# Kernel tuning notes

Measured on AMD Instinct MI355X. Metric: run time of the kernel, lower is better.

## Reference

```python
import jax, jax.numpy as jnp
import numpy as np

B, T, HID = 2, 1024, 2048
NH, NKV, HD = 16, 4, 128
L, INTER = 4, 5632
EPS = 1e-6


def _rope_tables(key):
    inv_freq = 1.0 / (10000.0 ** (jnp.arange(0, HD, 2, dtype=jnp.float32) / HD))  # [HD/2]
    pos = jnp.arange(T, dtype=jnp.float32)
    freqs = pos[:, None] * inv_freq[None, :]          # [T, HD/2]
    emb = jnp.concatenate([freqs, freqs], axis=-1)    # [T, HD]
    cos = jnp.broadcast_to(jnp.cos(emb)[None], (B, T, HD))
    sin = jnp.broadcast_to(jnp.sin(emb)[None], (B, T, HD))
    return cos, sin


def setup_inputs() -> dict:
    key = jax.random.key(0)
    ks = jax.random.split(key, 12)
    std = 0.02
    cos, sin = _rope_tables(key)
    return {
        "hidden_states": jax.random.normal(ks[0], (B, T, HID), jnp.float32),
        "cos": cos,
        "sin": sin,
        "qw": jax.random.normal(ks[1], (L, NH * HD, HID), jnp.float32) * std,
        "qb": jnp.zeros((L, NH * HD), jnp.float32),
        "kw": jax.random.normal(ks[2], (L, NKV * HD, HID), jnp.float32) * std,
        "kb": jnp.zeros((L, NKV * HD), jnp.float32),
        "vw": jax.random.normal(ks[3], (L, NKV * HD, HID), jnp.float32) * std,
        "vb": jnp.zeros((L, NKV * HD), jnp.float32),
        "ow": jax.random.normal(ks[4], (L, HID, NH * HD), jnp.float32) * std,
        "gatew": jax.random.normal(ks[5], (L, INTER, HID), jnp.float32) * std,
        "upw": jax.random.normal(ks[6], (L, INTER, HID), jnp.float32) * std,
        "downw": jax.random.normal(ks[7], (L, HID, INTER), jnp.float32) * std,
        "ln1w": jnp.ones((L, HID), jnp.float32),
        "ln2w": jnp.ones((L, HID), jnp.float32),
        "normw": jnp.ones((HID,), jnp.float32),
    }


def _rmsnorm(x, w):
    xf = x.astype(jnp.float32)
    var = jnp.mean(xf * xf, axis=-1, keepdims=True)
    return (w * (xf * jax.lax.rsqrt(var + EPS))).astype(x.dtype)


def _rotate_half(x):
    x1, x2 = x[..., : HD // 2], x[..., HD // 2:]
    return jnp.concatenate([-x2, x1], axis=-1)


def _layer(x, cos, sin, mask, qw, qb, kw, kb, vw, vb, ow, gw, uw, dw, l1, l2):
    # --- attention (PreNorm) ---
    h = _rmsnorm(x, l1)
    q = (h @ qw.T + qb).reshape(B, T, NH, HD).transpose(0, 2, 1, 3)    # [B,NH,T,D]
    k = (h @ kw.T + kb).reshape(B, T, NKV, HD).transpose(0, 2, 1, 3)   # [B,NKV,T,D]
    v = (h @ vw.T + vb).reshape(B, T, NKV, HD).transpose(0, 2, 1, 3)
    c, s = cos[:, None], sin[:, None]                                  # [B,1,T,D]
    q = q * c + _rotate_half(q) * s
    k = k * c + _rotate_half(k) * s
    rep = NH // NKV
    k = jnp.repeat(k, rep, axis=1)                                     # GQA repeat_kv
    v = jnp.repeat(v, rep, axis=1)
    scores = jnp.einsum("bhqd,bhkd->bhqk", q, k) / (HD ** 0.5) + mask
    attn = jax.nn.softmax(scores.astype(jnp.float32), axis=-1).astype(q.dtype)
    ao = jnp.einsum("bhqk,bhkd->bhqd", attn, v)
    ao = ao.transpose(0, 2, 1, 3).reshape(B, T, NH * HD) @ ow.T
    x = x + ao
    # --- SwiGLU MLP (PreNorm) ---
    h = _rmsnorm(x, l2)
    x = x + (jax.nn.silu(h @ gw.T) * (h @ uw.T)) @ dw.T
    return x


def reference(hidden_states, cos, sin, qw, qb, kw, kb, vw, vb, ow,
              gatew, upw, downw, ln1w, ln2w, normw):
    min_val = jnp.finfo(hidden_states.dtype).min
    qpos = jnp.arange(T)
    mask = jnp.where(qpos[None, :] > qpos[:, None], min_val, 0.0).astype(hidden_states.dtype)
    mask = mask[None, None]  # [1,1,T,T]
    x = hidden_states
    for i in range(L):
        x = _layer(x, cos, sin, mask, qw[i], qb[i], kw[i], kb[i], vw[i], vb[i],
                   ow[i], gatew[i], upw[i], downw[i], ln1w[i], ln2w[i])
    return _rmsnorm(x, normw)
```

## Files before the change

kernel.cpp:

```cpp
#include <hip/hip_runtime.h>


typedef __attribute__((ext_vector_type(8))) __bf16 bf16x8;
typedef __attribute__((ext_vector_type(4))) float f32x4;
typedef __attribute__((ext_vector_type(4))) unsigned short u16x4;

#define DEV __device__ __forceinline__
#define BARRIER() asm volatile("s_barrier" ::: "memory")

#define NTOK 2048
#define HIDDIM 2048
#define KVDIM 512
#define HDIM 128
#define INTERDIM 5632

DEV unsigned short f2bf(float f) {
  union { float f; unsigned u; } a; a.f = f;
  unsigned r = a.u + 0x7fffu + ((a.u >> 16) & 1u);
  return (unsigned short)(r >> 16);
}
DEV float bf2f(unsigned short h) {
  union { unsigned u; float f; } a; a.u = ((unsigned)h) << 16;
  return a.f;
}
DEV unsigned short f2h(float f) {
  union { _Float16 h; unsigned short u; } c; c.h = (_Float16)f; return c.u;
}
DEV float h2f(unsigned short u) {
  union { unsigned short u; _Float16 h; } c; c.u = u; return (float)c.h;
}
DEV void gload_lds16(const void* g, void* l) {
  __builtin_amdgcn_global_load_lds(
      (const __attribute__((address_space(1))) unsigned int*)(g),
      (__attribute__((address_space(3))) unsigned int*)(l), 16, 0, 0);
}

__global__ __launch_bounds__(256) void cvt_kernel(
    const float* __restrict__ in, unsigned short* __restrict__ out, int n8) {
  const int i = blockIdx.x * 256 + threadIdx.x;
  if (i >= n8) return;
  const f32x4* p = reinterpret_cast<const f32x4*>(in) + (size_t)i * 2;
  const f32x4 a = p[0], b = p[1];
  bf16x8 o;
  o[0] = (__bf16)a.x; o[1] = (__bf16)a.y; o[2] = (__bf16)a.z; o[3] = (__bf16)a.w;
  o[4] = (__bf16)b.x; o[5] = (__bf16)b.y; o[6] = (__bf16)b.z; o[7] = (__bf16)b.w;
  *reinterpret_cast<bf16x8*>(out + (size_t)i * 8) = o;
}

__global__ __launch_bounds__(256) void cvt_gu(
    const float* __restrict__ gw, const float* __restrict__ uw,
    unsigned short* __restrict__ out) {
  const int i = blockIdx.x * 256 + threadIdx.x;
  const int row = i >> 8, g8 = i & 255;
  const int t = row >> 8, sub = row & 255;
  const float* src = (sub < 128)
                         ? gw + (size_t)(t * 128 + sub) * 2048
                         : uw + (size_t)(t * 128 + sub - 128) * 2048;
  const f32x4* p = reinterpret_cast<const f32x4*>(src) + (size_t)g8 * 2;
  const f32x4 a = p[0], b = p[1];
  bf16x8 o;
  o[0] = (__bf16)a.x; o[1] = (__bf16)a.y; o[2] = (__bf16)a.z; o[3] = (__bf16)a.w;
  o[4] = (__bf16)b.x; o[5] = (__bf16)b.y; o[6] = (__bf16)b.z; o[7] = (__bf16)b.w;
  *reinterpret_cast<bf16x8*>(out + (size_t)row * 2048 + g8 * 8) = o;
}

template <int OUTF32>
__global__ __launch_bounds__(256) void rmsnorm_kernel(
    const float* __restrict__ x, const float* __restrict__ w,
    void* __restrict__ outp) {
  const int row = blockIdx.x, tid = threadIdx.x;
  const int lane = tid & 63, wave = tid >> 6;
  const float* xr = x + (size_t)row * HIDDIM;
  f32x4 v0 = *reinterpret_cast<const f32x4*>(xr + tid * 4);
  f32x4 v1 = *reinterpret_cast<const f32x4*>(xr + 1024 + tid * 4);
  float ss = v0.x * v0.x + v0.y * v0.y + v0.z * v0.z + v0.w * v0.w +
             v1.x * v1.x + v1.y * v1.y + v1.z * v1.z + v1.w * v1.w;
#pragma unroll
  for (int off = 1; off < 64; off <<= 1) ss += __shfl_xor(ss, off, 64);
  __shared__ float red[4];
  if (lane == 0) red[wave] = ss;
  __syncthreads();
  ss = red[0] + red[1] + red[2] + red[3];
  const float rs = rsqrtf(ss * (1.0f / 2048.0f) + 1e-6f);
  f32x4 w0 = *reinterpret_cast<const f32x4*>(w + tid * 4);
  f32x4 w1 = *reinterpret_cast<const f32x4*>(w + 1024 + tid * 4);
  if (OUTF32) {
    float* o = (float*)outp + (size_t)row * HIDDIM;
    f32x4 o0, o1;
    o0.x = v0.x * rs * w0.x; o0.y = v0.y * rs * w0.y;
    o0.z = v0.z * rs * w0.z; o0.w = v0.w * rs * w0.w;
    o1.x = v1.x * rs * w1.x; o1.y = v1.y * rs * w1.y;
    o1.z = v1.z * rs * w1.z; o1.w = v1.w * rs * w1.w;
    *reinterpret_cast<f32x4*>(o + tid * 4) = o0;
    *reinterpret_cast<f32x4*>(o + 1024 + tid * 4) = o1;
  } else {
    unsigned short* o = (unsigned short*)outp + (size_t)row * HIDDIM;
    u16x4 p0, p1;
    p0.x = f2bf(v0.x * rs * w0.x); p0.y = f2bf(v0.y * rs * w0.y);
    p0.z = f2bf(v0.z * rs * w0.z); p0.w = f2bf(v0.w * rs * w0.w);
    p1.x = f2bf(v1.x * rs * w1.x); p1.y = f2bf(v1.y * rs * w1.y);
    p1.z = f2bf(v1.z * rs * w1.z); p1.w = f2bf(v1.w * rs * w1.w);
    *reinterpret_cast<u16x4*>(o + tid * 4) = p0;
    *reinterpret_cast<u16x4*>(o + 1024 + tid * 4) = p1;
  }
}

template <int KS, int OUTF32>
__global__ __launch_bounds__(256) void reduce_rms(
    float* __restrict__ x, const unsigned short* __restrict__ p, size_t zs,
    const float* __restrict__ w, void* __restrict__ outp) {
  const int row = blockIdx.x, tid = threadIdx.x;
  const int lane = tid & 63, wave = tid >> 6;
  float* xr = x + (size_t)row * HIDDIM;
  f32x4 v0 = *reinterpret_cast<const f32x4*>(xr + tid * 4);
  f32x4 v1 = *reinterpret_cast<const f32x4*>(xr + 1024 + tid * 4);
#pragma unroll
  for (int s = 0; s < KS; ++s) {
    const unsigned short* pr = p + (size_t)s * zs + (size_t)row * HIDDIM;
    u16x4 a = *reinterpret_cast<const u16x4*>(pr + tid * 4);
    u16x4 b = *reinterpret_cast<const u16x4*>(pr + 1024 + tid * 4);
    v0.x += bf2f(a.x); v0.y += bf2f(a.y); v0.z += bf2f(a.z); v0.w += bf2f(a.w);
    v1.x += bf2f(b.x); v1.y += bf2f(b.y); v1.z += bf2f(b.z); v1.w += bf2f(b.w);
  }
  *reinterpret_cast<f32x4*>(xr + tid * 4) = v0;
  *reinterpret_cast<f32x4*>(xr + 1024 + tid * 4) = v1;
  float ss = v0.x * v0.x + v0.y * v0.y + v0.z * v0.z + v0.w * v0.w +
             v1.x * v1.x + v1.y * v1.y + v1.z * v1.z + v1.w * v1.w;
#pragma unroll
  for (int off = 1; off < 64; off <<= 1) ss += __shfl_xor(ss, off, 64);
  __shared__ float red[4];
  if (lane == 0) red[wave] = ss;
  __syncthreads();
  ss = red[0] + red[1] + red[2] + red[3];
  const float rs = rsqrtf(ss * (1.0f / 2048.0f) + 1e-6f);
  f32x4 w0 = *reinterpret_cast<const f32x4*>(w + tid * 4);
  f32x4 w1 = *reinterpret_cast<const f32x4*>(w + 1024 + tid * 4);
  if (OUTF32) {
    float* o = (float*)outp + (size_t)row * HIDDIM;
    f32x4 o0, o1;
    o0.x = v0.x * rs * w0.x; o0.y = v0.y * rs * w0.y;
    o0.z = v0.z * rs * w0.z; o0.w = v0.w * rs * w0.w;
    o1.x = v1.x * rs * w1.x; o1.y = v1.y * rs * w1.y;
    o1.z = v1.z * rs * w1.z; o1.w = v1.w * rs * w1.w;
    *reinterpret_cast<f32x4*>(o + tid * 4) = o0;
    *reinterpret_cast<f32x4*>(o + 1024 + tid * 4) = o1;
  } else {
    unsigned short* o = (unsigned short*)outp + (size_t)row * HIDDIM;
    u16x4 p0, p1;
    p0.x = f2bf(v0.x * rs * w0.x); p0.y = f2bf(v0.y * rs * w0.y);
    p0.z = f2bf(v0.z * rs * w0.z); p0.w = f2bf(v0.w * rs * w0.w);
    p1.x = f2bf(v1.x * rs * w1.x); p1.y = f2bf(v1.y * rs * w1.y);
    p1.z = f2bf(v1.z * rs * w1.z); p1.w = f2bf(v1.w * rs * w1.w);
    *reinterpret_cast<u16x4*>(o + tid * 4) = p0;
    *reinterpret_cast<u16x4*>(o + 1024 + tid * 4) = p1;
  }
}

struct G16Setup {
  const unsigned short* srcp0;
  const unsigned short* srcp1;
  int ldsc0, ldsc1;
};

DEV G16Setup g16_setup(const unsigned short* A, const unsigned short* W,
                       int K, int m0, int n0, int t0, int wave, int lane) {
  const int c0 = wave * 2, c1 = wave * 2 + 1;
  const int rA = lane >> 2;
  const int cg = (((lane & 3) ^ ((lane >> 3) & 3))) * 8;
  G16Setup s;
  const unsigned short* gb[4] = {
      A + (size_t)m0 * K, A + (size_t)(m0 + 128) * K,
      W + (size_t)n0 * K, W + (size_t)(n0 + 128) * K};
  s.srcp0 = gb[c0 >> 3] + (size_t)((c0 & 7) * 16 + rA) * K + cg +
            (size_t)t0 * 32;
  s.srcp1 = gb[c1 >> 3] + (size_t)((c1 & 7) * 16 + rA) * K + cg +
            (size_t)t0 * 32;
  s.ldsc0 = c0 * 512;
  s.ldsc1 = c1 * 512;
  return s;
}

#define G16STAGE(st_, tt_, c_)                                                \
  do {                                                                        \
    gload_lds16(st_.srcp0 + (size_t)(tt_)*32, &lds[(c_)*16384 + st_.ldsc0]);  \
    gload_lds16(st_.srcp1 + (size_t)(tt_)*32, &lds[(c_)*16384 + st_.ldsc1]);  \
  } while (0)

#define G16LDA(mi_, c_)                                                       \
  (*reinterpret_cast<const bf16x8*>(                                          \
      &lds[(c_)*16384 + (wm >> 1) * 4096 +                                    \
           (((wm & 1) * 64) + (mi_)*16 + fr) * 32 +                           \
           ((lq ^ ((fr >> 1) & 3))) * 8]))
#define G16LDB(ni_, c_)                                                       \
  (*reinterpret_cast<const bf16x8*>(                                          \
      &lds[(c_)*16384 + (2 + (wn >> 1)) * 4096 +                              \
           (((wn & 1) * 64) + (ni_)*16 + fr) * 32 +                           \
           ((lq ^ ((fr >> 1) & 3))) * 8]))

#define G16KLOOP(NT_)                                                         \
  G16STAGE(st, 0, 0);                                                         \
  for (int t = 0; t < (NT_); ++t) {                                           \
    const int c = t & 1;                                                      \
    if (t + 1 < (NT_)) {                                                      \
      G16STAGE(st, t + 1, c ^ 1);                                             \
      asm volatile("s_waitcnt vmcnt(2)" ::: "memory");                        \
    } else {                                                                  \
      asm volatile("s_waitcnt vmcnt(0)" ::: "memory");                        \
    }                                                                         \
    BARRIER();                                                                \
    bf16x8 aF[4], bF[4];                                                      \
    bF[0] = G16LDB(0, c); bF[1] = G16LDB(1, c);                               \
    bF[2] = G16LDB(2, c); bF[3] = G16LDB(3, c);                               \
    aF[0] = G16LDA(0, c); aF[1] = G16LDA(1, c);                               \
    aF[2] = G16LDA(2, c); aF[3] = G16LDA(3, c);                               \
    __builtin_amdgcn_s_setprio(1);                                            \
    _Pragma("unroll") for (int ni = 0; ni < 4; ++ni)                          \
        _Pragma("unroll") for (int mi = 0; mi < 4; ++mi)                      \
            acc[mi][ni] = __builtin_amdgcn_mfma_f32_16x16x32_bf16(            \
                aF[mi], bF[ni], acc[mi][ni], 0, 0, 0);                        \
    __builtin_amdgcn_s_setprio(0);                                            \
    __builtin_amdgcn_sched_barrier(0);                                        \
    BARRIER();                                                                \
  }

__global__ __launch_bounds__(1024) void gemm16w(
    const unsigned short* __restrict__ A, const unsigned short* __restrict__ W,
    unsigned short* __restrict__ outp, int K, int ldo, int kt_split,
    int kt_tot, size_t zstride) {
  __shared__ unsigned short lds[32768];
  const int tid = threadIdx.x, lane = tid & 63, wave = tid >> 6;
  const int fr = lane & 15, lq = lane >> 4;
  const int wm = wave >> 2, wn = wave & 3;

  int bx = blockIdx.x, by = blockIdx.y;
  {
    const int nbx = gridDim.x, nwg = nbx * gridDim.y;
    const int lin = by * nbx + bx, cpx = nwg >> 3;
    const int swz = (lin & 7) * cpx + (lin >> 3);
    bx = swz % nbx; by = swz / nbx;
  }
  const int m0 = by * 256, n0 = bx * 256;
  const int bz = blockIdx.z;
  const int t0 = bz * kt_split;
  int NT = kt_tot - t0; if (NT > kt_split) NT = kt_split;

  G16Setup st = g16_setup(A, W, K, m0, n0, t0, wave, lane);
  f32x4 acc[4][4] = {};
  G16KLOOP(NT);

  const int r0 = lq * 4;
#pragma unroll
  for (int mi = 0; mi < 4; ++mi)
#pragma unroll
    for (int ni = 0; ni < 4; ++ni)
#pragma unroll
      for (int r = 0; r < 4; ++r) {
        const int gm = m0 + wm * 64 + mi * 16 + r0 + r;
        const int gn = n0 + wn * 64 + ni * 16 + fr;
        outp[(size_t)bz * zstride + (size_t)gm * ldo + gn] =
            f2bf(acc[mi][ni][r]);
      }
}

__global__ __launch_bounds__(1024) void gemm_gu16(
    const unsigned short* __restrict__ A, const unsigned short* __restrict__ W,
    unsigned short* __restrict__ act) {
  __shared__ unsigned short lds[32768];
  const int tid = threadIdx.x, lane = tid & 63, wave = tid >> 6;
  const int fr = lane & 15, lq = lane >> 4;
  const int wm = wave >> 2, wn = wave & 3;
  const int K = 2048;

  int bx = blockIdx.x, by = blockIdx.y;
  {
    const int nbx = gridDim.x, nwg = nbx * gridDim.y;
    const int lin = by * nbx + bx, cpx = nwg >> 3;
    const int swz = (lin & 7) * cpx + (lin >> 3);
    bx = swz % nbx; by = swz / nbx;
  }
  const int m0 = by * 256, n0 = bx * 256;

  G16Setup st = g16_setup(A, W, K, m0, n0, 0, wave, lane);
  f32x4 acc[4][4] = {};
  G16KLOOP(64);

  float* fl = reinterpret_cast<float*>(lds);
  const int r0 = lq * 4;
#pragma unroll 1
  for (int rd = 0; rd < 4; ++rd) {
    __syncthreads();
    if (wm == rd && wn < 2) {
#pragma unroll
      for (int mi = 0; mi < 4; ++mi)
#pragma unroll
        for (int ni = 0; ni < 4; ++ni)
#pragma unroll
          for (int r = 0; r < 4; ++r)
            fl[(mi * 16 + r0 + r) * 128 + wn * 64 + ni * 16 + fr] =
                acc[mi][ni][r];
    }
    __syncthreads();
    if (wm == rd && wn >= 2) {
      const int wnu = wn - 2;
#pragma unroll
      for (int mi = 0; mi < 4; ++mi)
#pragma unroll
        for (int ni = 0; ni < 4; ++ni)
#pragma unroll
          for (int r = 0; r < 4; ++r) {
            const int mrow = mi * 16 + r0 + r;
            const float g = fl[mrow * 128 + wnu * 64 + ni * 16 + fr];
            const float s = g / (1.f + __expf(-g));
            const int gm = m0 + wm * 64 + mrow;
            const int ic = (n0 >> 1) + wnu * 64 + ni * 16 + fr;
            act[(size_t)gm * INTERDIM + ic] = f2bf(s * acc[mi][ni][r]);
          }
    }
  }
}

template <int MB>
DEV void mfma16(const bf16x8 (&aF)[4], const bf16x8 (&bF)[4],
                f32x4 (&acc)[8][4]) {
#pragma unroll
  for (int ni = 0; ni < 4; ++ni)
#pragma unroll
    for (int mi = 0; mi < 4; ++mi)
      acc[MB + mi][ni] = __builtin_amdgcn_mfma_f32_16x16x32_bf16(
          aF[mi], bF[ni], acc[MB + mi][ni], 0, 0, 0);
}

__global__ __launch_bounds__(512, 2) void gemm_qk(
    const unsigned short* __restrict__ q, const unsigned short* __restrict__ k,
    unsigned short* __restrict__ s) {
  __shared__ unsigned short lds[65536];
  const int tid = threadIdx.x, lane = tid & 63, wave = tid >> 6;
  const int fr = lane & 15, lq = lane >> 4;
  const int wm = wave >> 2, wn = wave & 3;

  int bx = blockIdx.x, by = blockIdx.y;
  {
    const int nbx = gridDim.x, nwg = nbx * gridDim.y;
    const int lin = by * nbx + bx, cpx = nwg >> 3;
    const int swz = (lin & 7) * cpx + (lin >> 3);
    bx = swz % nbx; by = swz / nbx;
  }
  if (bx > by) return;
  const int z = blockIdx.z, b = z >> 4, h = z & 15, kvh = h >> 2;
  const unsigned short* A = q + (size_t)b * 1024 * HIDDIM + h * HDIM;
  const unsigned short* W = k + (size_t)b * 1024 * KVDIM + kvh * HDIM;
  unsigned short* outp = s + (size_t)z * 1048576;
  const int m0 = by * 256, n0 = bx * 256;

  const int u0 = tid, u1 = tid + 512;
  const int r0s = u0 >> 3, r1s = u1 >> 3;
  const int c0 = ((u0 & 7) ^ (r0s & 7)) << 3, c1 = ((u1 & 7) ^ (r1s & 7)) << 3;
  const size_t offA0 = (size_t)r0s * HIDDIM + c0;
  const size_t offA1 = (size_t)r1s * HIDDIM + c1;
  const size_t offW0 = (size_t)r0s * KVDIM + c0;
  const size_t offW1 = (size_t)r1s * KVDIM + c1;
  const unsigned short* gb0 = A + (size_t)m0 * HIDDIM;
  const unsigned short* gb1 = A + (size_t)(m0 + 128) * HIDDIM;
  const unsigned short* gb2 = W + (size_t)n0 * KVDIM;
  const unsigned short* gb3 = W + (size_t)(n0 + 128) * KVDIM;

#define QSTAGE(h_, tt_, b_)                                                   \
  do {                                                                        \
    const unsigned short* _g =                                                \
        ((h_) == 0 ? gb0 : (h_) == 1 ? gb1 : (h_) == 2 ? gb2 : gb3) +         \
        (size_t)(tt_)*64;                                                     \
    const size_t _o0 = (h_) < 2 ? offA0 : offW0;                              \
    const size_t _o1 = (h_) < 2 ? offA1 : offW1;                              \
    unsigned short* _l = &lds[(b_)*32768 + (h_)*8192 + wave * 512];           \
    gload_lds16(_g + _o0, _l);                                                \
    gload_lds16(_g + _o1, _l + 4096);                                         \
  } while (0)

  const int e0 = lq ^ (fr & 7);
  const int cbA = wm * 8192;
  const int cbB = (2 + (wn >> 1)) * 8192;
  const int rB0 = (wn & 1) * 64 + fr;

#define QLDA(mi_, ks_, c_)                                                    \
  (*reinterpret_cast<const bf16x8*>(                                          \
      &lds[(c_)*32768 + cbA + ((mi_)*16 + fr) * 64 + ((e0 ^ ((ks_)*4)) << 3)]))
#define QLDB(ni_, ks_, c_)                                                    \
  (*reinterpret_cast<const bf16x8*>(                                          \
      &lds[(c_)*32768 + cbB + (rB0 + (ni_)*16) * 64 + ((e0 ^ ((ks_)*4)) << 3)]))

  f32x4 acc[8][4] = {};
  bf16x8 aF[4], bF[4];

  QSTAGE(0, 0, 0); QSTAGE(1, 0, 0); QSTAGE(2, 0, 0); QSTAGE(3, 0, 0);

  for (int t = 0; t < 2; ++t) {
    const int c = t & 1;
    if (t == 0) {
      QSTAGE(0, 1, 1); QSTAGE(2, 1, 1);
      asm volatile("s_waitcnt vmcnt(4)" ::: "memory");
    } else {
      asm volatile("s_waitcnt vmcnt(0)" ::: "memory");
    }
    BARRIER();
    bF[0] = QLDB(0, 0, c); bF[1] = QLDB(1, 0, c);
    bF[2] = QLDB(2, 0, c); bF[3] = QLDB(3, 0, c);
    aF[0] = QLDA(0, 0, c); aF[1] = QLDA(1, 0, c);
    aF[2] = QLDA(2, 0, c); aF[3] = QLDA(3, 0, c);
    if (t == 0) { QSTAGE(1, 1, 1); QSTAGE(3, 1, 1); }
    BARRIER();
    __builtin_amdgcn_s_setprio(1);
    mfma16<0>(aF, bF, acc);
    __builtin_amdgcn_s_setprio(0);
    __builtin_amdgcn_sched_barrier(0);
    BARRIER();
    aF[0] = QLDA(4, 0, c); aF[1] = QLDA(5, 0, c);
    aF[2] = QLDA(6, 0, c); aF[3] = QLDA(7, 0, c);
    BARRIER();
    __builtin_amdgcn_s_setprio(1);
    mfma16<4>(aF, bF, acc);
    __builtin_amdgcn_s_setprio(0);
    __builtin_amdgcn_sched_barrier(0);
    BARRIER();
    bF[0] = QLDB(0, 1, c); bF[1] = QLDB(1, 1, c);
    bF[2] = QLDB(2, 1, c); bF[3] = QLDB(3, 1, c);
    aF[0] = QLDA(0, 1, c); aF[1] = QLDA(1, 1, c);
    aF[2] = QLDA(2, 1, c); aF[3] = QLDA(3, 1, c);
    BARRIER();
    __builtin_amdgcn_s_setprio(1);
    mfma16<0>(aF, bF, acc);
    __builtin_amdgcn_s_setprio(0);
    __builtin_amdgcn_sched_barrier(0);
    BARRIER();
    aF[0] = QLDA(4, 1, c); aF[1] = QLDA(5, 1, c);
    aF[2] = QLDA(6, 1, c); aF[3] = QLDA(7, 1, c);
    BARRIER();
    __builtin_amdgcn_s_setprio(1);
    mfma16<4>(aF, bF, acc);
    __builtin_amdgcn_s_setprio(0);
    __builtin_amdgcn_sched_barrier(0);
    BARRIER();
  }

  const float scale = 0.08838834764831845f;
  const int r0 = lq * 4;
#pragma unroll
  for (int mi = 0; mi < 8; ++mi)
#pragma unroll
    for (int ni = 0; ni < 4; ++ni)
#pragma unroll
      for (int r = 0; r < 4; ++r) {
        const int gm = m0 + wm * 128 + mi * 16 + r0 + r;
        const int gn = n0 + wn * 64 + ni * 16 + fr;
        outp[(size_t)gm * 1024 + gn] = f2h(acc[mi][ni][r] * scale);
      }
#undef QSTAGE
#undef QLDA
#undef QLDB
}

__global__ __launch_bounds__(256) void softmax_rows(unsigned short* __restrict__ s) {
  const int row = blockIdx.x, tid = threadIdx.x;
  const int lane = tid & 63, wave = tid >> 6;
  const int qv = row & 1023;
  const int nact = ((qv >> 8) + 1) << 8;
  unsigned short* r = s + (size_t)row * 1024;
  const int col = tid * 4;
  const bool act = (col < nact);
  float v[4];
  if (act) {
    u16x4 raw = *reinterpret_cast<const u16x4*>(r + col);
#pragma unroll
    for (int j = 0; j < 4; ++j)
      v[j] = (col + j <= qv) ? h2f(((unsigned short*)&raw)[j]) : -1e30f;
  } else {
#pragma unroll
    for (int j = 0; j < 4; ++j) v[j] = -1e30f;
  }
  float mx = fmaxf(fmaxf(v[0], v[1]), fmaxf(v[2], v[3]));
#pragma unroll
  for (int off = 1; off < 64; off <<= 1) mx = fmaxf(mx, __shfl_xor(mx, off, 64));
  __shared__ float redm[4], reds[4];
  if (lane == 0) redm[wave] = mx;
  __syncthreads();
  const float M = fmaxf(fmaxf(redm[0], redm[1]), fmaxf(redm[2], redm[3]));
  float e[4], ts = 0.f;
#pragma unroll
  for (int j = 0; j < 4; ++j) {
    e[j] = (act && col + j <= qv) ? __expf(v[j] - M) : 0.f;
    ts += e[j];
  }
#pragma unroll
  for (int off = 1; off < 64; off <<= 1) ts += __shfl_xor(ts, off, 64);
  if (lane == 0) reds[wave] = ts;
  __syncthreads();
  const float inv = 1.f / (reds[0] + reds[1] + reds[2] + reds[3]);
  if (act) {
    u16x4 o;
    o.x = f2bf(e[0] * inv); o.y = f2bf(e[1] * inv);
    o.z = f2bf(e[2] * inv); o.w = f2bf(e[3] * inv);
    *reinterpret_cast<u16x4*>(r + col) = o;
  }
}

__global__ __launch_bounds__(256, 2) void gemm_pv(
    const unsigned short* __restrict__ p, const unsigned short* __restrict__ vt,
    unsigned short* __restrict__ ao) {
  __shared__ unsigned short lds[40960];
  const int tid = threadIdx.x, lane = tid & 63, wave = tid >> 6;
  const int fr = lane & 15, lq = lane >> 4;
  const int bxn = blockIdx.x, by = blockIdx.y, z = blockIdx.z;
  const int b = z >> 4, h = z & 15, kvh = h >> 2;
  const int m0p = by * 256, n0 = bxn * 64;
  const int NT = by * 4 + 4;

  const unsigned short* A = p + (size_t)z * 1048576 + (size_t)m0p * 1024;
  const unsigned short* W =
      vt + ((size_t)(b * 4 + kvh) * 128 + n0) * 1024;

#define PVSTAGE(tt_, c_)                                                      \
  do {                                                                        \
    _Pragma("unroll")                                                         \
    for (int j = 0; j < 8; ++j) {                                             \
      const int u = wave * 512 + j * 64 + lane;                               \
      const int rw = u >> 3;                                                  \
      gload_lds16(A + (size_t)rw * 1024 + (((u & 7) ^ (rw & 7)) << 3) +       \
                      (size_t)(tt_)*64,                                       \
                  &lds[(c_)*20480 + wave * 4096 + j * 512]);                  \
    }                                                                         \
    _Pragma("unroll")                                                         \
    for (int j = 0; j < 2; ++j) {                                             \
      const int u = wave * 128 + j * 64 + lane;                               \
      const int rw = u >> 3;                                                  \
      gload_lds16(W + (size_t)rw * 1024 + (((u & 7) ^ (rw & 7)) << 3) +       \
                      (size_t)(tt_)*64,                                       \
                  &lds[(c_)*20480 + 16384 + wave * 1024 + j * 512]);          \
    }                                                                         \
  } while (0)

  const int e0 = lq ^ (fr & 7);
#define PVLDA(mi_, ks_, c_)                                                   \
  (*reinterpret_cast<const bf16x8*>(                                          \
      &lds[(c_)*20480 + (wave * 64 + (mi_)*16 + fr) * 64 +                    \
           ((e0 ^ ((ks_)*4)) << 3)]))
#define PVLDB(ni_, ks_, c_)                                                   \
  (*reinterpret_cast<const bf16x8*>(                                          \
      &lds[(c_)*20480 + 16384 + ((ni_)*16 + fr) * 64 +                        \
           ((e0 ^ ((ks_)*4)) << 3)]))

  f32x4 acc[4][4] = {};
  bf16x8 aF[4], bF[4];

  PVSTAGE(0, 0);

  for (int t = 0; t < NT; ++t) {
    const int c = t & 1;
    if (t + 1 < NT) {
      PVSTAGE(t + 1, c ^ 1);
      asm volatile("s_waitcnt vmcnt(10)" ::: "memory");
    } else {
      asm volatile("s_waitcnt vmcnt(0)" ::: "memory");
    }
    BARRIER();
#pragma unroll
    for (int ks = 0; ks < 2; ++ks) {
      bF[0] = PVLDB(0, ks, c); bF[1] = PVLDB(1, ks, c);
      bF[2] = PVLDB(2, ks, c); bF[3] = PVLDB(3, ks, c);
      aF[0] = PVLDA(0, ks, c); aF[1] = PVLDA(1, ks, c);
      aF[2] = PVLDA(2, ks, c); aF[3] = PVLDA(3, ks, c);
      BARRIER();
      __builtin_amdgcn_s_setprio(1);
#pragma unroll
      for (int ni = 0; ni < 4; ++ni)
#pragma unroll
        for (int mi = 0; mi < 4; ++mi)
          acc[mi][ni] = __builtin_amdgcn_mfma_f32_16x16x32_bf16(
              aF[mi], bF[ni], acc[mi][ni], 0, 0, 0);
      __builtin_amdgcn_s_setprio(0);
      __builtin_amdgcn_sched_barrier(0);
      BARRIER();
    }
  }

  const int r0 = lq * 4;
#pragma unroll
  for (int mi = 0; mi < 4; ++mi)
#pragma unroll
    for (int ni = 0; ni < 4; ++ni)
#pragma unroll
      for (int r = 0; r < 4; ++r) {
        const int gm = m0p + wave * 64 + mi * 16 + r0 + r;
        const int gn = n0 + ni * 16 + fr;
        ao[(size_t)(b * 1024 + gm) * HIDDIM + h * HDIM + gn] =
            f2bf(acc[mi][ni][r]);
      }
#undef PVSTAGE
#undef PVLDA
#undef PVLDB
}

__global__ __launch_bounds__(256) void reduce_qkv(
    const unsigned short* __restrict__ p, const float* __restrict__ qb,
    const float* __restrict__ kb, const float* __restrict__ vb,
    const float* __restrict__ cosb, const float* __restrict__ sinb,
    unsigned short* __restrict__ qo, unsigned short* __restrict__ ko,
    unsigned short* __restrict__ vto) {
  const int i = blockIdx.x * 256 + threadIdx.x;
  const int row = i / 768, c4 = (i - row * 768) * 4;
  const unsigned short* p0 = p + (size_t)row * 3072;
  const unsigned short* p1 = p + 6291456 + (size_t)row * 3072;
  const u16x4 a0 = *reinterpret_cast<const u16x4*>(p0 + c4);
  const u16x4 a1 = *reinterpret_cast<const u16x4*>(p1 + c4);
  f32x4 s;
  s.x = bf2f(a0.x) + bf2f(a1.x); s.y = bf2f(a0.y) + bf2f(a1.y);
  s.z = bf2f(a0.z) + bf2f(a1.z); s.w = bf2f(a0.w) + bf2f(a1.w);
  if (c4 < 2560) {
    const float* bias; unsigned short* out; int d, ldo;
    if (c4 < 2048) { bias = qb; out = qo; d = c4;        ldo = HIDDIM; }
    else           { bias = kb; out = ko; d = c4 - 2048; ldo = KVDIM; }
    const int dd = d & 127;
    const bool lohalf = (dd < 64);
    const int pc = lohalf ? c4 + 64 : c4 - 64;
    const int pd = lohalf ? d + 64 : d - 64;
    const u16x4 b0 = *reinterpret_cast<const u16x4*>(p0 + pc);
    const u16x4 b1 = *reinterpret_cast<const u16x4*>(p1 + pc);
    f32x4 sp;
    sp.x = bf2f(b0.x) + bf2f(b1.x); sp.y = bf2f(b0.y) + bf2f(b1.y);
    sp.z = bf2f(b0.z) + bf2f(b1.z); sp.w = bf2f(b0.w) + bf2f(b1.w);
    const f32x4 bv = *reinterpret_cast<const f32x4*>(bias + d);
    const f32x4 bp = *reinterpret_cast<const f32x4*>(bias + pd);
    const f32x4 cv = *reinterpret_cast<const f32x4*>(cosb + (size_t)row * 128 + dd);
    const f32x4 sv = *reinterpret_cast<const f32x4*>(sinb + (size_t)row * 128 + dd);
    const f32x4 xv = s + bv, pv = sp + bp;
    f32x4 o;
    if (lohalf) o = xv * cv - pv * sv;
    else        o = xv * cv + pv * sv;
    u16x4 ob;
    ob.x = f2bf(o.x); ob.y = f2bf(o.y); ob.z = f2bf(o.z); ob.w = f2bf(o.w);
    *reinterpret_cast<u16x4*>(out + (size_t)row * ldo + d) = ob;
  } else {
    const int d = c4 - 2560;
    const int kvh = d >> 7, dd = d & 127;
    const int b = row >> 10, t = row & 1023;
    const f32x4 bv = *reinterpret_cast<const f32x4*>(vb + d);
    const f32x4 o = s + bv;
    unsigned short* vr =
        vto + ((size_t)(b * 4 + kvh) * 128 + dd) * 1024 + t;
    vr[0] = f2bf(o.x); vr[1024] = f2bf(o.y);
    vr[2048] = f2bf(o.z); vr[3072] = f2bf(o.w);
  }
}

extern "C" void kernel_launch(void* const* d_in, const int* in_sizes, int n_in,
                              void* d_out, int out_size, void* d_ws,
                              size_t ws_size, hipStream_t stream) {
  (void)in_sizes; (void)n_in; (void)out_size; (void)ws_size;
  const float* hidden = (const float*)d_in[0];
  const float* cosb  = (const float*)d_in[1];
  const float* sinb  = (const float*)d_in[2];
  const float* qw    = (const float*)d_in[3];
  const float* qbias = (const float*)d_in[4];
  const float* kw    = (const float*)d_in[5];
  const float* kbias = (const float*)d_in[6];
  const float* vw    = (const float*)d_in[7];
  const float* vbias = (const float*)d_in[8];
  const float* ow    = (const float*)d_in[9];
  const float* gw    = (const float*)d_in[10];
  const float* uw    = (const float*)d_in[11];
  const float* dw    = (const float*)d_in[12];
  const float* ln1   = (const float*)d_in[13];
  const float* ln2   = (const float*)d_in[14];
  const float* normw = (const float*)d_in[15];

  char* ws = (char*)d_ws;
  float* x               = (float*)ws;
  unsigned short* hbuf   = (unsigned short*)(ws + 16777216);
  unsigned short* qbuf   = (unsigned short*)(ws + 25165824);
  unsigned short* kbuf   = (unsigned short*)(ws + 33554432);
  unsigned short* vtbuf  = (unsigned short*)(ws + 35651584);
  unsigned short* aobuf  = (unsigned short*)(ws + 39845888);
  unsigned short* actbuf = (unsigned short*)(ws + 71303168);
  unsigned short* wcvt   = (unsigned short*)(ws + 94371840);
  unsigned short* pbQKV = (unsigned short*)(ws + 37748736);
  unsigned short* sbuf  = (unsigned short*)(ws + 48234496);
  unsigned short* pbO   = (unsigned short*)(ws + 48234496);
  unsigned short* wgu   = (unsigned short*)(ws + 25165824);
  unsigned short* pbD   = (unsigned short*)(ws + 25165824);

  unsigned short* wq16 = wcvt;
  unsigned short* wk16 = wcvt + 4194304;
  unsigned short* wv16 = wcvt + 5242880;
  unsigned short* ow16 = wcvt;

  hipMemcpyAsync(x, hidden, (size_t)NTOK * HIDDIM * 4,
                 hipMemcpyDeviceToDevice, stream);
  rmsnorm_kernel<0><<<NTOK, 256, 0, stream>>>(x, ln1, hbuf);

  for (int l = 0; l < 4; ++l) {
    const float* qw_l = qw + (size_t)l * 2048 * 2048;
    const float* qb_l = qbias + (size_t)l * 2048;
    const float* kw_l = kw + (size_t)l * 512 * 2048;
    const float* kb_l = kbias + (size_t)l * 512;
    const float* vw_l = vw + (size_t)l * 512 * 2048;
    const float* vb_l = vbias + (size_t)l * 512;
    const float* ow_l = ow + (size_t)l * 2048 * 2048;
    const float* gw_l = gw + (size_t)l * 5632 * 2048;
    const float* uw_l = uw + (size_t)l * 5632 * 2048;
    const float* dw_l = dw + (size_t)l * 2048 * 5632;

    cvt_kernel<<<2048, 256, 0, stream>>>(qw_l, wq16, 524288);
    cvt_kernel<<<512, 256, 0, stream>>>(kw_l, wk16, 131072);
    cvt_kernel<<<512, 256, 0, stream>>>(vw_l, wv16, 131072);
    gemm16w<<<dim3(12, 8, 2), 1024, 0, stream>>>(
        hbuf, wcvt, pbQKV, 2048, 3072, 32, 64, (size_t)6291456);
    reduce_qkv<<<6144, 256, 0, stream>>>(pbQKV, qb_l, kb_l, vb_l, cosb, sinb,
                                         qbuf, kbuf, vtbuf);

    gemm_qk<<<dim3(4, 4, 32), 512, 0, stream>>>(qbuf, kbuf, sbuf);
    softmax_rows<<<32768, 256, 0, stream>>>(sbuf);
    gemm_pv<<<dim3(2, 4, 32), 256, 0, stream>>>(sbuf, vtbuf, aobuf);

    cvt_kernel<<<2048, 256, 0, stream>>>(ow_l, ow16, 524288);
    gemm16w<<<dim3(8, 8, 4), 1024, 0, stream>>>(
        aobuf, ow16, pbO, 2048, 2048, 16, 64, (size_t)4194304);
    reduce_rms<4, 0><<<NTOK, 256, 0, stream>>>(x, pbO, (size_t)4194304,
                                               ln2 + l * 2048, hbuf);

    cvt_gu<<<11264, 256, 0, stream>>>(gw_l, uw_l, wgu);
    gemm_gu16<<<dim3(44, 8), 1024, 0, stream>>>(hbuf, wgu, actbuf);

    cvt_kernel<<<5632, 256, 0, stream>>>(dw_l, wcvt, 1441792);
    gemm16w<<<dim3(8, 8, 4), 1024, 0, stream>>>(
        actbuf, wcvt, pbD, 5632, 2048, 44, 176, (size_t)4194304);
    if (l < 3) {
      reduce_rms<4, 0><<<NTOK, 256, 0, stream>>>(
          x, pbD, (size_t)4194304, ln1 + (l + 1) * 2048, hbuf);
    } else {
      reduce_rms<4, 1><<<NTOK, 256, 0, stream>>>(x, pbD, (size_t)4194304,
                                                 normw, d_out);
    }
  }
}
```

Measured before the change: 1.661 ms.

## Rewrite gate/up GEMM as 512-thread double-buffered kernel with column-major XCD swizzle

The fused gate/up SwiGLU GEMM moves from a 1024-thread, 16-wave kernel to a 512-thread kernel that allows two blocks per CU. Each wave now computes 128x64 outputs over K-steps of 64, with double-buffered LDS staging through global_load_lds. The SiLU epilogue runs in one LDS pass instead of four serialized rounds. A shared XCD block-swizzle helper now walks the grid column-major (by = swz % nby) and is also used by gemm16w and gemm_qk, which changes tile ordering and cache locality in those kernels too. The costs are more registers per wave (128 accumulators), 128KB of LDS per block, and possible occupancy or spill pressure.

```diff
diff --git a/kernel.cpp b/kernel.cpp
--- a/kernel.cpp
+++ b/kernel.cpp
@@ -33,6 +33,15 @@
   __builtin_amdgcn_global_load_lds(
       (const __attribute__((address_space(1))) unsigned int*)(g),
       (__attribute__((address_space(3))) unsigned int*)(l), 16, 0, 0);
+}
+
+DEV void xcd_decode(int& bx, int& by) {
+  const int nbx = gridDim.x, nby = gridDim.y;
+  const int nwg = nbx * nby;
+  const int lin = by * nbx + bx, cpx = nwg >> 3;
+  const int swz = (lin & 7) * cpx + (lin >> 3);
+  by = swz % nby;
+  bx = swz / nby;
 }
 
 __global__ __launch_bounds__(256) void cvt_kernel(
@@ -156,6 +165,17 @@
   }
 }
 
+template <int MB>
+DEV void mfma16(const bf16x8 (&aF)[4], const bf16x8 (&bF)[4],
+                f32x4 (&acc)[8][4]) {
+#pragma unroll
+  for (int ni = 0; ni < 4; ++ni)
+#pragma unroll
+    for (int mi = 0; mi < 4; ++mi)
+      acc[MB + mi][ni] = __builtin_amdgcn_mfma_f32_16x16x32_bf16(
+          aF[mi], bF[ni], acc[MB + mi][ni], 0, 0, 0);
+}
+
 struct G16Setup {
   const unsigned short* srcp0;
   const unsigned short* srcp1;
@@ -233,12 +253,7 @@
   const int wm = wave >> 2, wn = wave & 3;
 
   int bx = blockIdx.x, by = blockIdx.y;
-  {
-    const int nbx = gridDim.x, nwg = nbx * gridDim.y;
-    const int lin = by * nbx + bx, cpx = nwg >> 3;
-    const int swz = (lin & 7) * cpx + (lin >> 3);
-    bx = swz % nbx; by = swz / nbx;
-  }
+  xcd_decode(bx, by);
   const int m0 = by * 256, n0 = bx * 256;
   const int bz = blockIdx.z;
   const int t0 = bz * kt_split;
@@ -262,72 +277,137 @@
       }
 }
 
-__global__ __launch_bounds__(1024) void gemm_gu16(
+__global__ __launch_bounds__(512, 2) void gemm_gu(
     const unsigned short* __restrict__ A, const unsigned short* __restrict__ W,
     unsigned short* __restrict__ act) {
-  __shared__ unsigned short lds[32768];
+  __shared__ unsigned short lds[65536];
   const int tid = threadIdx.x, lane = tid & 63, wave = tid >> 6;
   const int fr = lane & 15, lq = lane >> 4;
   const int wm = wave >> 2, wn = wave & 3;
   const int K = 2048;
 
   int bx = blockIdx.x, by = blockIdx.y;
-  {
-    const int nbx = gridDim.x, nwg = nbx * gridDim.y;
-    const int lin = by * nbx + bx, cpx = nwg >> 3;
-    const int swz = (lin & 7) * cpx + (lin >> 3);
-    bx = swz % nbx; by = swz / nbx;
-  }
+  xcd_decode(bx, by);
   const int m0 = by * 256, n0 = bx * 256;
 
-  G16Setup st = g16_setup(A, W, K, m0, n0, 0, wave, lane);
-  f32x4 acc[4][4] = {};
-  G16KLOOP(64);
+  const int u0 = tid, u1 = tid + 512;
+  const int r0s = u0 >> 3, r1s = u1 >> 3;
+  const size_t off0 = (size_t)r0s * K + (size_t)((((u0 & 7) ^ (r0s & 7))) << 3);
+  const size_t off1 = (size_t)r1s * K + (size_t)((((u1 & 7) ^ (r1s & 7))) << 3);
+  const unsigned short* gb0 = A + (size_t)(m0)*K;
+  const unsigned short* gb1 = A + (size_t)(m0 + 128) * K;
+  const unsigned short* gb2 = W + (size_t)(n0)*K;
+  const unsigned short* gb3 = W + (size_t)(n0 + 128) * K;
+
+#define STAGE(h_, tt_, b_)                                                    \
+  do {                                                                        \
+    const unsigned short* _g =                                                \
+        ((h_) == 0 ? gb0 : (h_) == 1 ? gb1 : (h_) == 2 ? gb2 : gb3) +         \
+        (size_t)(tt_)*64;                                                     \
+    unsigned short* _l = &lds[(b_)*32768 + (h_)*8192 + wave * 512];           \
+    gload_lds16(_g + off0, _l);                                               \
+    gload_lds16(_g + off1, _l + 4096);                                        \
+  } while (0)
+
+  const int e0 = lq ^ (fr & 7);
+  const int cbA = wm * 8192;
+  const int cbB = (2 + (wn >> 1)) * 8192;
+  const int rB0 = (wn & 1) * 64 + fr;
+
+#define LDA(mi_, ks_, c_)                                                     \
+  (*reinterpret_cast<const bf16x8*>(                                          \
+      &lds[(c_)*32768 + cbA + ((mi_)*16 + fr) * 64 + ((e0 ^ ((ks_)*4)) << 3)]))
+#define LDB(ni_, ks_, c_)                                                     \
+  (*reinterpret_cast<const bf16x8*>(                                          \
+      &lds[(c_)*32768 + cbB + (rB0 + (ni_)*16) * 64 + ((e0 ^ ((ks_)*4)) << 3)]))
+
+  f32x4 acc[8][4] = {};
+  bf16x8 aF[4], bF[4];
+
+  STAGE(0, 0, 0); STAGE(1, 0, 0); STAGE(2, 0, 0); STAGE(3, 0, 0);
+
+  for (int t = 0; t < 32; ++t) {
+    const int c = t & 1;
+    if (t + 1 < 32) {
+      STAGE(0, t + 1, c ^ 1);
+      STAGE(2, t + 1, c ^ 1);
+      asm volatile("s_waitcnt vmcnt(4)" ::: "memory");
+    } else {
+      asm volatile("s_waitcnt vmcnt(0)" ::: "memory");
+    }
+    BARRIER();
+    bF[0] = LDB(0, 0, c); bF[1] = LDB(1, 0, c);
+    bF[2] = LDB(2, 0, c); bF[3] = LDB(3, 0, c);
+    aF[0] = LDA(0, 0, c); aF[1] = LDA(1, 0, c);
+    aF[2] = LDA(2, 0, c); aF[3] = LDA(3, 0, c);
+    if (t + 1 < 32) { STAGE(1, t + 1, c ^ 1); STAGE(3, t + 1, c ^ 1); }
+    BARRIER();
+    __builtin_amdgcn_s_setprio(1);
+    mfma16<0>(aF, bF, acc);
+    __builtin_amdgcn_s_setprio(0);
+    __builtin_amdgcn_sched_barrier(0);
+    BARRIER();
+    aF[0] = LDA(4, 0, c); aF[1] = LDA(5, 0, c);
+    aF[2] = LDA(6, 0, c); aF[3] = LDA(7, 0, c);
+    BARRIER();
+    __builtin_amdgcn_s_setprio(1);
+    mfma16<4>(aF, bF, acc);
+    __builtin_amdgcn_s_setprio(0);
+    __builtin_amdgcn_sched_barrier(0);
+    BARRIER();
+    bF[0] = LDB(0, 1, c); bF[1] = LDB(1, 1, c);
+    bF[2] = LDB(2, 1, c); bF[3] = LDB(3, 1, c);
+    aF[0] = LDA(0, 1, c); aF[1] = LDA(1, 1, c);
+    aF[2] = LDA(2, 1, c); aF[3] = LDA(3, 1, c);
+    BARRIER();
+    __builtin_amdgcn_s_setprio(1);
+    mfma16<0>(aF, bF, acc);
+    __builtin_amdgcn_s_setprio(0);
+    __builtin_amdgcn_sched_barrier(0);
+    BARRIER();
+    aF[0] = LDA(4, 1, c); aF[1] = LDA(5, 1, c);
+    aF[2] = LDA(6, 1, c); aF[3] = LDA(7, 1, c);
+    BARRIER();
+    __builtin_amdgcn_s_setprio(1);
+    mfma16<4>(aF, bF, acc);
+    __builtin_amdgcn_s_setprio(0);
+    __builtin_amdgcn_sched_barrier(0);
+    BARRIER();
+  }
 
   float* fl = reinterpret_cast<float*>(lds);
   const int r0 = lq * 4;
-#pragma unroll 1
-  for (int rd = 0; rd < 4; ++rd) {
-    __syncthreads();
-    if (wm == rd && wn < 2) {
-#pragma unroll
-      for (int mi = 0; mi < 4; ++mi)
-#pragma unroll
-        for (int ni = 0; ni < 4; ++ni)
-#pragma unroll
-          for (int r = 0; r < 4; ++r)
-            fl[(mi * 16 + r0 + r) * 128 + wn * 64 + ni * 16 + fr] =
-                acc[mi][ni][r];
-    }
-    __syncthreads();
-    if (wm == rd && wn >= 2) {
-      const int wnu = wn - 2;
-#pragma unroll
-      for (int mi = 0; mi < 4; ++mi)
-#pragma unroll
-        for (int ni = 0; ni < 4; ++ni)
-#pragma unroll
-          for (int r = 0; r < 4; ++r) {
-            const int mrow = mi * 16 + r0 + r;
-            const float g = fl[mrow * 128 + wnu * 64 + ni * 16 + fr];
-            const float s = g / (1.f + __expf(-g));
-            const int gm = m0 + wm * 64 + mrow;
-            const int ic = (n0 >> 1) + wnu * 64 + ni * 16 + fr;
-            act[(size_t)gm * INTERDIM + ic] = f2bf(s * acc[mi][ni][r]);
-          }
-    }
-  }
-}
-
-template <int MB>
-DEV void mfma16(const bf16x8 (&aF)[4], const bf16x8 (&bF)[4],
-                f32x4 (&acc)[8][4]) {
-#pragma unroll
-  for (int ni = 0; ni < 4; ++ni)
-#pragma unroll
-    for (int mi = 0; mi < 4; ++mi)
-      acc[MB + mi][ni] = __builtin_amdgcn_mfma_f32_16x16x32_bf16(
-          aF[mi], bF[ni], acc[MB + mi][ni], 0, 0, 0);
+  __syncthreads();
+  if (wn < 2) {
+#pragma unroll
+    for (int mi = 0; mi < 8; ++mi)
+#pragma unroll
+      for (int ni = 0; ni < 4; ++ni)
+#pragma unroll
+        for (int r = 0; r < 4; ++r)
+          fl[wm * 16384 + (mi * 16 + r0 + r) * 128 + wn * 64 + ni * 16 + fr] =
+              acc[mi][ni][r];
+  }
+  __syncthreads();
+  if (wn >= 2) {
+    const int wnu = wn - 2;
+#pragma unroll
+    for (int mi = 0; mi < 8; ++mi)
+#pragma unroll
+      for (int ni = 0; ni < 4; ++ni)
+#pragma unroll
+        for (int r = 0; r < 4; ++r) {
+          const int mrow = mi * 16 + r0 + r;
+          const float gv = fl[wm * 16384 + mrow * 128 + wnu * 64 + ni * 16 + fr];
+          const float s = gv / (1.f + __expf(-gv));
+          const int gm = m0 + wm * 128 + mrow;
+          const int ic = (n0 >> 1) + wnu * 64 + ni * 16 + fr;
+          act[(size_t)gm * INTERDIM + ic] = f2bf(s * acc[mi][ni][r]);
+        }
+  }
+#undef STAGE
+#undef LDA
+#undef LDB
 }
 
 __global__ __launch_bounds__(512, 2) void gemm_qk(
@@ -339,12 +419,7 @@
   const int wm = wave >> 2, wn = wave & 3;
 
   int bx = blockIdx.x, by = blockIdx.y;
-  {
-    const int nbx = gridDim.x, nwg = nbx * gridDim.y;
-    const int lin = by * nbx + bx, cpx = nwg >> 3;
-    const int swz = (lin & 7) * cpx + (lin >> 3);
-    bx = swz % nbx; by = swz / nbx;
-  }
+  xcd_decode(bx, by);
   if (bx > by) return;
   const int z = blockIdx.z, b = z >> 4, h = z & 15, kvh = h >> 2;
   const unsigned short* A = q + (size_t)b * 1024 * HIDDIM + h * HDIM;
@@ -726,7 +801,7 @@
                                                ln2 + l * 2048, hbuf);
 
     cvt_gu<<<11264, 256, 0, stream>>>(gw_l, uw_l, wgu);
-    gemm_gu16<<<dim3(44, 8), 1024, 0, stream>>>(hbuf, wgu, actbuf);
+    gemm_gu<<<dim3(44, 8), 512, 0, stream>>>(hbuf, wgu, actbuf);
 
     cvt_kernel<<<5632, 256, 0, stream>>>(dw_l, wcvt, 1441792);
     gemm16w<<<dim3(8, 8, 4), 1024, 0, stream>>>(
```

After: 1.619 ms. 2.5% less time.
